# Kernel tuning notes

Measured on AMD Instinct MI355X. Metric: run time of the kernel, lower is better.

The kernel has to match this reference:

```python
import jax, jax.numpy as jnp
import numpy as np

B, S, D, H = 2, 2048, 768, 12
HD = D // H


def setup_inputs() -> dict:
    key = jax.random.key(0)
    ks = jax.random.split(key, 8)
    scale = 1.0 / np.sqrt(D)
    inp = {
        "q": jax.random.normal(ks[0], (B, S, D), jnp.float32),
        "k": jax.random.normal(ks[1], (B, S, D), jnp.float32),
        "v": jax.random.normal(ks[2], (B, S, D), jnp.float32),
        # causal mask: 1.0 where attention is disallowed (upper triangle)
        "mask": jnp.triu(jnp.ones((S, S), jnp.float32), k=1)[None, None, :, :],
        "Wq": jax.random.normal(ks[3], (D, D), jnp.float32) * scale,
        "bq": jnp.zeros((D,), jnp.float32),
        "Wk": jax.random.normal(ks[4], (D, D), jnp.float32) * scale,
        "bk": jnp.zeros((D,), jnp.float32),
        "Wv": jax.random.normal(ks[5], (D, D), jnp.float32) * scale,
        "bv": jnp.zeros((D,), jnp.float32),
        "Wo": jax.random.normal(ks[6], (D, D), jnp.float32) * scale,
        "bo": jnp.zeros((D,), jnp.float32),
    }
    return inp


def _split_heads(x):
    # [B, S, D] -> [B, H, S, HD]
    b, s, _ = x.shape
    return x.reshape(b, s, H, HD).transpose(0, 2, 1, 3)


def reference(q, k, v, mask, Wq, bq, Wk, bk, Wv, bv, Wo, bo):
    qh = _split_heads(q @ Wq + bq)
    kh = _split_heads(k @ Wk + bk)
    vh = _split_heads(v @ Wv + bv)
    scale = 1.0 / jnp.sqrt(jnp.asarray(HD, qh.dtype))
    # [B, H, Sq, Sk] — full attention matrix, as in the original
    scores = jnp.einsum("bhqd,bhkd->bhqk", qh, kh) * scale
    scores = scores + mask * -1e9
    attn = jax.nn.softmax(scores, axis=-1)  # dropout is identity at inference
    out = jnp.einsum("bhqk,bhkd->bhqd", attn, vh)
    out = out.transpose(0, 2, 1, 3).reshape(q.shape[0], -1, D)
    return out @ Wo + bo
```

## Files before the change

### kernel.cpp

```cpp
#include <hip/hip_runtime.h>

#define SEQ    2048
#define NB     2
#define DMODEL 768
#define NH     12
#define HDIM   64
#define BS     (NB * SEQ)

typedef __bf16  bf16x8  __attribute__((ext_vector_type(8)));
typedef ushort  ushort8 __attribute__((ext_vector_type(8)));
typedef float   floatx4 __attribute__((ext_vector_type(4)));

#define GLOBAL_AS __attribute__((address_space(1)))
#define LDS_AS    __attribute__((address_space(3)))

union PackU8 { ushort u[8]; uint4 v; };
union PackU4 { ushort u[4]; uint2 v; };

__device__ __forceinline__ ushort f2bf(float x) {
    union { float f; unsigned u; } t; t.f = x;
    unsigned r = t.u + 0x7fffu + ((t.u >> 16) & 1u);
    return (ushort)(r >> 16);
}

__device__ __forceinline__ bf16x8 ld_frag(const ushort* p) {
    return __builtin_bit_cast(bf16x8, *(const ushort8*)p);
}

__global__ void convert_x(const float* __restrict__ q, const float* __restrict__ k,
                          const float* __restrict__ v,
                          ushort* __restrict__ qo, ushort* __restrict__ ko,
                          ushort* __restrict__ vo)
{
    const float* src = blockIdx.z == 0 ? q : blockIdx.z == 1 ? k : v;
    ushort*      dst = blockIdx.z == 0 ? qo : blockIdx.z == 1 ? ko : vo;
    const int i = (blockIdx.x * 256 + threadIdx.x) * 4;
    const float4 f = *(const float4*)(src + i);
    ushort4 o;
    o.x = f2bf(f.x); o.y = f2bf(f.y); o.z = f2bf(f.z); o.w = f2bf(f.w);
    *(ushort4*)(dst + i) = o;
}

__global__ __launch_bounds__(256)
void convert_wT(const float* __restrict__ wq, const float* __restrict__ wk,
                const float* __restrict__ wv, const float* __restrict__ wo,
                ushort* __restrict__ wtcat, ushort* __restrict__ wto)
{
    __shared__ float Tf[64][69];
    const int z = blockIdx.z;
    const float* w = z == 0 ? wq : z == 1 ? wk : z == 2 ? wv : wo;
    ushort*      o = z < 3 ? wtcat + (size_t)z * DMODEL * DMODEL : wto;
    const int k0 = blockIdx.x * 64, n0 = blockIdx.y * 64;
    const int tid = threadIdx.x;
#pragma unroll
    for (int p = 0; p < 4; ++p) {
        const int idx = tid + p * 256;
        const int r = idx >> 4, c = (idx & 15) * 4;
        const float4 f = *(const float4*)&w[(size_t)(k0 + r) * DMODEL + n0 + c];
        Tf[r][c] = f.x; Tf[r][c + 1] = f.y; Tf[r][c + 2] = f.z; Tf[r][c + 3] = f.w;
    }
    __syncthreads();
#pragma unroll
    for (int p = 0; p < 2; ++p) {
        const int idx = tid + p * 256;
        const int n = idx >> 3, kk = (idx & 7) * 8;
        PackU8 pk;
#pragma unroll
        for (int j = 0; j < 8; ++j) pk.u[j] = f2bf(Tf[kk + j][n]);
        *(uint4*)&o[(size_t)(n0 + n) * DMODEL + k0 + kk] = pk.v;
    }
}

__global__ __launch_bounds__(256)
void gemm_qkv(const ushort* __restrict__ xq, const ushort* __restrict__ xk,
              const ushort* __restrict__ xv, const ushort* __restrict__ WT,
              const float* __restrict__ bq, const float* __restrict__ bk,
              const float* __restrict__ bv,
              ushort* __restrict__ oq, ushort* __restrict__ ok,
              ushort* __restrict__ ov)
{
    __shared__ __align__(16) ushort As[128 * 32];
    __shared__ __align__(16) ushort Bs[128 * 32];

    const int z = blockIdx.y / 6;
    const ushort* X = z == 0 ? xq : z == 1 ? xk : xv;

    const int tid  = threadIdx.x;
    const int lane = tid & 63;
    const int w    = tid >> 6;
    const int l15  = lane & 15;
    const int quad = lane >> 4;
    const int wm   = (w >> 1) * 64;
    const int wn   = (w & 1) * 64;
    const int row0 = blockIdx.x * 128;
    const int col0 = blockIdx.y * 128;

    floatx4 acc[4][4];
    const floatx4 fzero = {0.f, 0.f, 0.f, 0.f};
#pragma unroll
    for (int i = 0; i < 4; ++i)
#pragma unroll
        for (int j = 0; j < 4; ++j) acc[i][j] = fzero;

    const int rin = lane >> 2;
    const int gc  = (lane & 3) * 8;

    for (int k0 = 0; k0 < DMODEL; k0 += 32) {
#pragma unroll
        for (int p = 0; p < 2; ++p) {
            const int ch = w * 2 + p;
            const int r  = ch * 16 + rin;
            __builtin_amdgcn_global_load_lds(
                (const GLOBAL_AS uint*)&X[(size_t)(row0 + r) * DMODEL + k0 + gc],
                (LDS_AS uint*)&As[ch * 512], 16, 0, 0);
            __builtin_amdgcn_global_load_lds(
                (const GLOBAL_AS uint*)&WT[(size_t)(col0 + r) * DMODEL + k0 + gc],
                (LDS_AS uint*)&Bs[ch * 512], 16, 0, 0);
        }
        __syncthreads();

        bf16x8 af[4], bfr[4];
#pragma unroll
        for (int t = 0; t < 4; ++t) {
            af[t]  = ld_frag(&As[(wm + t * 16 + l15) * 32 + quad * 8]);
            bfr[t] = ld_frag(&Bs[(wn + t * 16 + l15) * 32 + quad * 8]);
        }
#pragma unroll
        for (int ti = 0; ti < 4; ++ti)
#pragma unroll
            for (int tj = 0; tj < 4; ++tj)
                acc[ti][tj] = __builtin_amdgcn_mfma_f32_16x16x32_bf16(
                    af[ti], bfr[tj], acc[ti][tj], 0, 0, 0);
        __syncthreads();
    }

    const int c0 = (blockIdx.y % 6) * 128;
    const float*  bias = z == 0 ? bq : z == 1 ? bk : bv;
    ushort*       out  = z == 0 ? oq : z == 1 ? ok : ov;
    const float   sc   = (z == 0) ? 0.18033688f : 1.f;
#pragma unroll
    for (int tj = 0; tj < 4; ++tj) {
        const int c_l = c0 + wn + tj * 16 + l15;
        const float bb = bias[c_l];
        const int h  = c_l >> 6;
        const int dd = c_l & 63;
#pragma unroll
        for (int ti = 0; ti < 4; ++ti) {
#pragma unroll
            for (int ri = 0; ri < 4; ++ri) {
                const int r_g = row0 + wm + ti * 16 + quad * 4 + ri;
                const int b   = r_g >> 11;
                const int s   = r_g & (SEQ - 1);
                out[(((size_t)(b * NH + h) * SEQ + s) << 6) + dd] =
                    f2bf((acc[ti][tj][ri] + bb) * sc);
            }
        }
    }
}

__global__ __launch_bounds__(256)
void gemm_out(const ushort* __restrict__ X, const ushort* __restrict__ WT,
              const float* __restrict__ bias, float* __restrict__ fo)
{
    __shared__ __align__(16) ushort As[64][40];
    __shared__ __align__(16) ushort Bs[128][40];

    const int tid  = threadIdx.x;
    const int lane = tid & 63;
    const int wv   = tid >> 6;
    const int wm   = (wv >> 1) * 32;
    const int wn   = (wv & 1) * 64;
    const int l15  = lane & 15;
    const int quad = lane >> 4;
    const int row0 = blockIdx.x * 64;
    const int col0 = blockIdx.y * 128;

    floatx4 acc[2][4];
    const floatx4 fzero = {0.f, 0.f, 0.f, 0.f};
#pragma unroll
    for (int i = 0; i < 2; ++i)
#pragma unroll
        for (int j = 0; j < 4; ++j) acc[i][j] = fzero;

    const int sr = tid >> 2;
    const int sc = (tid & 3) * 8;

    for (int k0 = 0; k0 < DMODEL; k0 += 32) {
        *(uint4*)&As[sr][sc] = *(const uint4*)&X[(size_t)(row0 + sr) * DMODEL + k0 + sc];
#pragma unroll
        for (int p = 0; p < 2; ++p) {
            const int r = sr + p * 64;
            *(uint4*)&Bs[r][sc] = *(const uint4*)&WT[(size_t)(col0 + r) * DMODEL + k0 + sc];
        }
        __syncthreads();

        bf16x8 af[2], bfr[4];
#pragma unroll
        for (int t = 0; t < 2; ++t)
            af[t] = ld_frag(&As[wm + t * 16 + l15][quad * 8]);
#pragma unroll
        for (int t = 0; t < 4; ++t)
            bfr[t] = ld_frag(&Bs[wn + t * 16 + l15][quad * 8]);
#pragma unroll
        for (int ti = 0; ti < 2; ++ti)
#pragma unroll
            for (int tj = 0; tj < 4; ++tj)
                acc[ti][tj] = __builtin_amdgcn_mfma_f32_16x16x32_bf16(
                    af[ti], bfr[tj], acc[ti][tj], 0, 0, 0);
        __syncthreads();
    }

#pragma unroll
    for (int tj = 0; tj < 4; ++tj) {
        const int c_g = col0 + wn + tj * 16 + l15;
        const float bb = bias[c_g];
#pragma unroll
        for (int ti = 0; ti < 2; ++ti)
#pragma unroll
            for (int ri = 0; ri < 4; ++ri) {
                const int r_g = row0 + wm + ti * 16 + quad * 4 + ri;
                fo[(size_t)r_g * DMODEL + c_g] = acc[ti][tj][ri] + bb;
            }
    }
}

__global__ void transpose_v(const ushort* __restrict__ vh, ushort* __restrict__ vt)
{
    __shared__ __align__(16) ushort T[64][72];
    const int bh = blockIdx.y;
    const int s0 = blockIdx.x * 64;
    const ushort* src = vh + (size_t)bh * SEQ * HDIM;
    ushort*       dst = vt + (size_t)bh * HDIM * SEQ;

#pragma unroll
    for (int p = 0; p < 2; ++p) {
        const int idx = threadIdx.x + p * 256;
        const int r = idx >> 3, c = (idx & 7) * 8;
        *(uint4*)&T[r][c] = *(const uint4*)&src[(size_t)(s0 + r) * HDIM + c];
    }
    __syncthreads();
#pragma unroll
    for (int p = 0; p < 2; ++p) {
        const int idx = threadIdx.x + p * 256;
        const int d = idx >> 3, c = (idx & 7) * 8;
        PackU8 pk;
#pragma unroll
        for (int j = 0; j < 8; ++j) pk.u[j] = T[c + j][d];
        *(uint4*)&dst[(size_t)d * SEQ + s0 + c] = pk.v;
    }
}

__global__ __launch_bounds__(128)
void attn_mfma(const ushort* __restrict__ qh, const ushort* __restrict__ kh,
               const ushort* __restrict__ vt, ushort* __restrict__ ctx)
{
    __shared__ __align__(16) ushort Ks[2][64][64];
    __shared__ __align__(16) ushort Vs[2][64][64];
    __shared__ __align__(16) ushort Ps[32][64];

    const int tid  = threadIdx.x;
    const int lane = tid & 63;
    const int wv   = tid >> 6;
    const int l15  = lane & 15;
    const int quad = lane >> 4;
    const int e3   = l15 & 7;

    const int id  = blockIdx.x;
    const int xcd = id & 7;
    const int jj  = id >> 3;
    const int g   = jj >> 6;
    const int qt  = 63 - (jj & 63);
    const int bh  = xcd + 8 * g;
    const int b   = bh / NH, h = bh - b * NH;
    const int nk  = (qt >> 1) + 1;
    const size_t base = (size_t)bh * SEQ * HDIM;

    bf16x8 qf[2];
#pragma unroll
    for (int ks = 0; ks < 2; ++ks)
        qf[ks] = ld_frag(&qh[base + (size_t)(qt * 32 + wv * 16 + l15) * HDIM + ks * 32 + quad * 8]);
    asm volatile("s_waitcnt vmcnt(0)" ::: "memory");

    const int srow = lane >> 3;
    const int kcol = ((lane & 7) ^ (srow & 7)) * 8;

    auto stage = [&](int bufi, int c0s) {
#pragma unroll
        for (int p = 0; p < 4; ++p) {
            const int r = p * 16 + wv * 8 + srow;
            __builtin_amdgcn_global_load_lds(
                (const GLOBAL_AS uint*)&kh[base + (size_t)(c0s + r) * HDIM + kcol],
                (LDS_AS uint*)&Ks[bufi][p * 16 + wv * 8][0], 16, 0, 0);
            __builtin_amdgcn_global_load_lds(
                (const GLOBAL_AS uint*)&vt[base + (size_t)r * SEQ + c0s + kcol],
                (LDS_AS uint*)&Vs[bufi][p * 16 + wv * 8][0], 16, 0, 0);
        }
    };

    stage(0, 0);
    if (nk > 1) stage(1, 64);

    float l = 0.f;
    floatx4 O[4];
    const floatx4 fzero = {0.f, 0.f, 0.f, 0.f};
#pragma unroll
    for (int dj = 0; dj < 4; ++dj) O[dj] = fzero;

    const int row_g = qt * 32 + wv * 16 + l15;

    for (int t = 0; t < nk; ++t) {
        const int  cur  = t & 1;
        const int  c0   = t * 64;
        const bool diag = (t == nk - 1);

        if (t + 1 < nk) asm volatile("s_waitcnt vmcnt(8)" ::: "memory");
        else            asm volatile("s_waitcnt vmcnt(0)" ::: "memory");
        __builtin_amdgcn_s_barrier();

        bf16x8 kf[4][2], vf[4][2];
#pragma unroll
        for (int nj = 0; nj < 4; ++nj)
#pragma unroll
            for (int ks = 0; ks < 2; ++ks) {
                kf[nj][ks] = ld_frag(&Ks[cur][nj * 16 + l15][(ks * 32 + quad * 8) ^ (e3 << 3)]);
                vf[nj][ks] = ld_frag(&Vs[cur][nj * 16 + l15][(ks * 32 + quad * 8) ^ (e3 << 3)]);
            }

        if (t + 2 < nk) {
            asm volatile("s_waitcnt lgkmcnt(0)" ::: "memory");
            __builtin_amdgcn_s_barrier();
            stage(cur, (t + 2) * 64);
        }

        floatx4 S[4];
        __builtin_amdgcn_s_setprio(1);
#pragma unroll
        for (int nj = 0; nj < 4; ++nj) {
            S[nj] = __builtin_amdgcn_mfma_f32_16x16x32_bf16(kf[nj][0], qf[0], fzero, 0, 0, 0);
            S[nj] = __builtin_amdgcn_mfma_f32_16x16x32_bf16(kf[nj][1], qf[1], S[nj], 0, 0, 0);
        }
        __builtin_amdgcn_s_setprio(0);

        float rs = 0.f;
#pragma unroll
        for (int nj = 0; nj < 4; ++nj) {
            PackU4 pk;
#pragma unroll
            for (int ri = 0; ri < 4; ++ri) {
                const int krow = c0 + nj * 16 + quad * 4 + ri;
                float p = __builtin_amdgcn_exp2f(S[nj][ri]);
                if (diag && krow > row_g) p = 0.f;
                rs += p;
                union { float f; unsigned u; } tb; tb.f = p;
                pk.u[ri] = (ushort)(tb.u >> 16);
            }
            *(uint2*)&Ps[wv * 16 + l15][(nj * 16 + quad * 4) ^ (e3 << 3)] = pk.v;
        }
        rs += __shfl_xor(rs, 16);
        rs += __shfl_xor(rs, 32);
        l += rs;

        bf16x8 pf[2];
#pragma unroll
        for (int ks = 0; ks < 2; ++ks)
            pf[ks] = ld_frag(&Ps[wv * 16 + l15][(ks * 32 + quad * 8) ^ (e3 << 3)]);

        __builtin_amdgcn_s_setprio(1);
#pragma unroll
        for (int dj = 0; dj < 4; ++dj)
#pragma unroll
            for (int ks = 0; ks < 2; ++ks)
                O[dj] = __builtin_amdgcn_mfma_f32_16x16x32_bf16(pf[ks], vf[dj][ks], O[dj], 0, 0, 0);
        __builtin_amdgcn_s_setprio(0);
    }

    const float inv = 1.f / l;
    float ib[4];
#pragma unroll
    for (int ri = 0; ri < 4; ++ri) ib[ri] = __shfl(inv, quad * 4 + ri);
#pragma unroll
    for (int dj = 0; dj < 4; ++dj)
#pragma unroll
        for (int ri = 0; ri < 4; ++ri) {
            const int row = qt * 32 + wv * 16 + quad * 4 + ri;
            ctx[((size_t)b * SEQ + row) * DMODEL + h * HDIM + dj * 16 + l15] =
                f2bf(O[dj][ri] * ib[ri]);
        }
}

extern "C" void kernel_launch(void* const* d_in, const int* in_sizes, int n_in,
                              void* d_out, int out_size, void* d_ws, size_t ws_size,
                              hipStream_t stream)
{
    const float* q  = (const float*)d_in[0];
    const float* k  = (const float*)d_in[1];
    const float* v  = (const float*)d_in[2];
    const float* Wq = (const float*)d_in[4];
    const float* bq = (const float*)d_in[5];
    const float* Wk = (const float*)d_in[6];
    const float* bk = (const float*)d_in[7];
    const float* Wv = (const float*)d_in[8];
    const float* bv = (const float*)d_in[9];
    const float* Wo = (const float*)d_in[10];
    const float* bo = (const float*)d_in[11];
    float* out = (float*)d_out;

    char* ws = (char*)d_ws;
    const size_t ACT = (size_t)BS * DMODEL * 2;
    ushort* qx    = (ushort*)(ws);
    ushort* kx    = (ushort*)(ws + ACT);
    ushort* vx    = (ushort*)(ws + 2 * ACT);
    ushort* qhp   = (ushort*)(ws + 3 * ACT);
    ushort* khp   = (ushort*)(ws + 4 * ACT);
    ushort* vhp   = (ushort*)(ws + 5 * ACT);
    ushort* wtcat = (ushort*)(ws + 6 * ACT);
    ushort* wto   = wtcat + (size_t)3 * DMODEL * DMODEL;
    ushort* vhT   = vx;
    ushort* ctx   = qx;

    convert_x<<<dim3(BS * DMODEL / 1024, 1, 3), 256, 0, stream>>>(q, k, v, qx, kx, vx);
    convert_wT<<<dim3(12, 12, 4), 256, 0, stream>>>(Wq, Wk, Wv, Wo, wtcat, wto);
    gemm_qkv<<<dim3(BS / 128, 18), 256, 0, stream>>>(
        qx, kx, vx, wtcat, bq, bk, bv, qhp, khp, vhp);
    transpose_v<<<dim3(SEQ / 64, NB * NH), 256, 0, stream>>>(vhp, vhT);
    attn_mfma<<<dim3(1536), 128, 0, stream>>>(qhp, khp, vhT, ctx);
    gemm_out<<<dim3(BS / 64, DMODEL / 128), 256, 0, stream>>>(ctx, wto, bo, out);
}
```

Measured before the change: 199.0 us.

## Split attention tile across four waves, each handling half the keys and head dims

The attention kernel moves from 128 to 256 threads per block. Each pair of waves shares a 16-row query slice: one wave computes scores for half of the 64 keys and produces half of the output head dimensions. The P tile is exchanged through LDS with an extra barrier, and row sums are combined through a small shared reduction buffer. This is meant to raise parallelism and latency hiding per block. In exchange it adds barriers and per-wave synchronisation on P, and it changes the staging and prefetch order.

```diff
diff --git a/kernel.cpp b/kernel.cpp
--- a/kernel.cpp
+++ b/kernel.cpp
@@ -250,17 +250,20 @@
     }
 }
 
-__global__ __launch_bounds__(128)
+__global__ __launch_bounds__(256, 4)
 void attn_mfma(const ushort* __restrict__ qh, const ushort* __restrict__ kh,
                const ushort* __restrict__ vt, ushort* __restrict__ ctx)
 {
     __shared__ __align__(16) ushort Ks[2][64][64];
     __shared__ __align__(16) ushort Vs[2][64][64];
     __shared__ __align__(16) ushort Ps[32][64];
+    __shared__ float Lred[4][16];
 
     const int tid  = threadIdx.x;
     const int lane = tid & 63;
     const int wv   = tid >> 6;
+    const int qhf  = wv >> 1;
+    const int hf   = wv & 1;
     const int l15  = lane & 15;
     const int quad = lane >> 4;
     const int e3   = l15 & 7;
@@ -278,22 +281,22 @@
     bf16x8 qf[2];
 #pragma unroll
     for (int ks = 0; ks < 2; ++ks)
-        qf[ks] = ld_frag(&qh[base + (size_t)(qt * 32 + wv * 16 + l15) * HDIM + ks * 32 + quad * 8]);
+        qf[ks] = ld_frag(&qh[base + (size_t)(qt * 32 + qhf * 16 + l15) * HDIM + ks * 32 + quad * 8]);
     asm volatile("s_waitcnt vmcnt(0)" ::: "memory");
 
     const int srow = lane >> 3;
-    const int kcol = ((lane & 7) ^ (srow & 7)) * 8;
+    const int kcol = ((lane & 7) ^ srow) * 8;
 
     auto stage = [&](int bufi, int c0s) {
 #pragma unroll
-        for (int p = 0; p < 4; ++p) {
-            const int r = p * 16 + wv * 8 + srow;
+        for (int p = 0; p < 2; ++p) {
+            const int r = wv * 16 + p * 8 + srow;
             __builtin_amdgcn_global_load_lds(
                 (const GLOBAL_AS uint*)&kh[base + (size_t)(c0s + r) * HDIM + kcol],
-                (LDS_AS uint*)&Ks[bufi][p * 16 + wv * 8][0], 16, 0, 0);
+                (LDS_AS uint*)&Ks[bufi][wv * 16 + p * 8][0], 16, 0, 0);
             __builtin_amdgcn_global_load_lds(
                 (const GLOBAL_AS uint*)&vt[base + (size_t)r * SEQ + c0s + kcol],
-                (LDS_AS uint*)&Vs[bufi][p * 16 + wv * 8][0], 16, 0, 0);
+                (LDS_AS uint*)&Vs[bufi][wv * 16 + p * 8][0], 16, 0, 0);
         }
     };
 
@@ -301,90 +304,90 @@
     if (nk > 1) stage(1, 64);
 
     float l = 0.f;
-    floatx4 O[4];
+    floatx4 O[2];
     const floatx4 fzero = {0.f, 0.f, 0.f, 0.f};
-#pragma unroll
-    for (int dj = 0; dj < 4; ++dj) O[dj] = fzero;
-
-    const int row_g = qt * 32 + wv * 16 + l15;
+    O[0] = fzero; O[1] = fzero;
+
+    const int row_g = qt * 32 + qhf * 16 + l15;
 
     for (int t = 0; t < nk; ++t) {
         const int  cur  = t & 1;
         const int  c0   = t * 64;
         const bool diag = (t == nk - 1);
 
-        if (t + 1 < nk) asm volatile("s_waitcnt vmcnt(8)" ::: "memory");
+        if (t + 1 < nk) asm volatile("s_waitcnt vmcnt(4)" ::: "memory");
         else            asm volatile("s_waitcnt vmcnt(0)" ::: "memory");
         __builtin_amdgcn_s_barrier();
 
-        bf16x8 kf[4][2], vf[4][2];
-#pragma unroll
-        for (int nj = 0; nj < 4; ++nj)
+        bf16x8 kf[2][2], vf[2][2];
+#pragma unroll
+        for (int nl = 0; nl < 2; ++nl)
 #pragma unroll
             for (int ks = 0; ks < 2; ++ks) {
-                kf[nj][ks] = ld_frag(&Ks[cur][nj * 16 + l15][(ks * 32 + quad * 8) ^ (e3 << 3)]);
-                vf[nj][ks] = ld_frag(&Vs[cur][nj * 16 + l15][(ks * 32 + quad * 8) ^ (e3 << 3)]);
+                kf[nl][ks] = ld_frag(&Ks[cur][(2 * hf + nl) * 16 + l15][(ks * 32 + quad * 8) ^ (e3 << 3)]);
+                vf[nl][ks] = ld_frag(&Vs[cur][(2 * hf + nl) * 16 + l15][(ks * 32 + quad * 8) ^ (e3 << 3)]);
             }
 
-        if (t + 2 < nk) {
-            asm volatile("s_waitcnt lgkmcnt(0)" ::: "memory");
-            __builtin_amdgcn_s_barrier();
-            stage(cur, (t + 2) * 64);
-        }
-
-        floatx4 S[4];
+        floatx4 S[2];
         __builtin_amdgcn_s_setprio(1);
 #pragma unroll
-        for (int nj = 0; nj < 4; ++nj) {
-            S[nj] = __builtin_amdgcn_mfma_f32_16x16x32_bf16(kf[nj][0], qf[0], fzero, 0, 0, 0);
-            S[nj] = __builtin_amdgcn_mfma_f32_16x16x32_bf16(kf[nj][1], qf[1], S[nj], 0, 0, 0);
+        for (int nl = 0; nl < 2; ++nl) {
+            S[nl] = __builtin_amdgcn_mfma_f32_16x16x32_bf16(kf[nl][0], qf[0], fzero, 0, 0, 0);
+            S[nl] = __builtin_amdgcn_mfma_f32_16x16x32_bf16(kf[nl][1], qf[1], S[nl], 0, 0, 0);
         }
         __builtin_amdgcn_s_setprio(0);
 
         float rs = 0.f;
 #pragma unroll
-        for (int nj = 0; nj < 4; ++nj) {
+        for (int nl = 0; nl < 2; ++nl) {
             PackU4 pk;
 #pragma unroll
             for (int ri = 0; ri < 4; ++ri) {
-                const int krow = c0 + nj * 16 + quad * 4 + ri;
-                float p = __builtin_amdgcn_exp2f(S[nj][ri]);
+                const int krow = c0 + (2 * hf + nl) * 16 + quad * 4 + ri;
+                float p = __builtin_amdgcn_exp2f(S[nl][ri]);
                 if (diag && krow > row_g) p = 0.f;
                 rs += p;
                 union { float f; unsigned u; } tb; tb.f = p;
                 pk.u[ri] = (ushort)(tb.u >> 16);
             }
-            *(uint2*)&Ps[wv * 16 + l15][(nj * 16 + quad * 4) ^ (e3 << 3)] = pk.v;
+            *(uint2*)&Ps[qhf * 16 + l15][((2 * hf + nl) * 16 + quad * 4) ^ (e3 << 3)] = pk.v;
         }
         rs += __shfl_xor(rs, 16);
         rs += __shfl_xor(rs, 32);
         l += rs;
 
+        asm volatile("s_waitcnt lgkmcnt(0)" ::: "memory");
+        __builtin_amdgcn_s_barrier();
+        if (t + 2 < nk) stage(cur, (t + 2) * 64);
+
         bf16x8 pf[2];
 #pragma unroll
         for (int ks = 0; ks < 2; ++ks)
-            pf[ks] = ld_frag(&Ps[wv * 16 + l15][(ks * 32 + quad * 8) ^ (e3 << 3)]);
+            pf[ks] = ld_frag(&Ps[qhf * 16 + l15][(ks * 32 + quad * 8) ^ (e3 << 3)]);
 
         __builtin_amdgcn_s_setprio(1);
 #pragma unroll
-        for (int dj = 0; dj < 4; ++dj)
+        for (int dl = 0; dl < 2; ++dl)
 #pragma unroll
             for (int ks = 0; ks < 2; ++ks)
-                O[dj] = __builtin_amdgcn_mfma_f32_16x16x32_bf16(pf[ks], vf[dj][ks], O[dj], 0, 0, 0);
+                O[dl] = __builtin_amdgcn_mfma_f32_16x16x32_bf16(pf[ks], vf[dl][ks], O[dl], 0, 0, 0);
         __builtin_amdgcn_s_setprio(0);
     }
 
-    const float inv = 1.f / l;
+    if (quad == 0) Lred[wv][l15] = l;
+    __syncthreads();
+    const float lt  = Lred[qhf * 2][l15] + Lred[qhf * 2 + 1][l15];
+    const float inv = 1.f / lt;
     float ib[4];
 #pragma unroll
     for (int ri = 0; ri < 4; ++ri) ib[ri] = __shfl(inv, quad * 4 + ri);
 #pragma unroll
-    for (int dj = 0; dj < 4; ++dj)
+    for (int dl = 0; dl < 2; ++dl)
 #pragma unroll
         for (int ri = 0; ri < 4; ++ri) {
-            const int row = qt * 32 + wv * 16 + quad * 4 + ri;
-            ctx[((size_t)b * SEQ + row) * DMODEL + h * HDIM + dj * 16 + l15] =
-                f2bf(O[dj][ri] * ib[ri]);
+            const int row = qt * 32 + qhf * 16 + quad * 4 + ri;
+            ctx[((size_t)b * SEQ + row) * DMODEL + h * HDIM + (2 * hf + dl) * 16 + l15] =
+                f2bf(O[dl][ri] * ib[ri]);
         }
 }
 
@@ -423,6 +426,6 @@
     gemm_qkv<<<dim3(BS / 128, 18), 256, 0, stream>>>(
         qx, kx, vx, wtcat, bq, bk, bv, qhp, khp, vhp);
     transpose_v<<<dim3(SEQ / 64, NB * NH), 256, 0, stream>>>(vhp, vhT);
-    attn_mfma<<<dim3(1536), 128, 0, stream>>>(qhp, khp, vhT, ctx);
+    attn_mfma<<<dim3(1536), 256, 0, stream>>>(qhp, khp, vhT, ctx);
     gemm_out<<<dim3(BS / 64, DMODEL / 128), 256, 0, stream>>>(ctx, wto, bo, out);
 }
```

Result: no change. 198.6 us, median of 2 (-0.2%).
